# Kernel tuning notes

Measured on AMD Instinct MI355X. Metric: run time of the kernel, lower is better.

The kernel has to match this reference:

```python
import jax, jax.numpy as jnp
import numpy as np

C = 256
P = 8          # partition_size
DH = 32        # dim_head
NH = C // DH   # num heads
EXP = 4        # mlp expansion
EPS = 1e-5


def conv2d(x, w, b, stride, pad, groups):
    # x: NCHW, w: (O, I/groups, kh, kw)
    y = jax.lax.conv_general_dilated(
        x, w, (stride, stride), [(pad, pad), (pad, pad)],
        dimension_numbers=('NCHW', 'OIHW', 'NCHW'), feature_group_count=groups)
    return y + b[None, :, None, None]


def layernorm(x, g, b):
    m = jnp.mean(x, axis=-1, keepdims=True)
    v = jnp.mean((x - m) ** 2, axis=-1, keepdims=True)
    return (x - m) * jax.lax.rsqrt(v + EPS) * g + b


def partition_block(x):
    # (B,H,W,C) -> (B*nH*nW, P, P, C), MaxViT 'block' mode
    B, H, W, c = x.shape
    x = x.reshape(B, H // P, P, W // P, P, c)
    return x.transpose(0, 1, 3, 2, 4, 5).reshape(-1, P, P, c)


def reverse_block(w, H, W):
    c = w.shape[-1]
    x = w.reshape(-1, H // P, W // P, P, P, c)
    return x.transpose(0, 1, 3, 2, 4, 5).reshape(-1, H, W, c)


def window_attn(xw, qkv_w, qkv_b, proj_w, proj_b):
    # xw: (Nw, P, P, C); faithful to SelfAttentionCl (dropout inactive at eval)
    Nw = xw.shape[0]
    L = P * P
    qkv = xw.reshape(Nw, L, C) @ qkv_w.T + qkv_b           # (Nw, L, 3C)
    qkv = qkv.reshape(Nw, L, NH, 3 * DH).transpose(0, 2, 1, 3)  # (Nw, nh, L, 3dh)
    q, k, v = jnp.split(qkv, 3, axis=-1)
    attn = jax.nn.softmax((q @ jnp.swapaxes(k, -1, -2)) * (DH ** -0.5), axis=-1)
    o = (attn @ v).transpose(0, 2, 1, 3).reshape(Nw, P, P, C)
    return o @ proj_w.T + proj_b


def setup_inputs() -> dict:
    key = jax.random.key(0)
    ks = jax.random.split(key, 16)
    s = 0.02
    d = {
        'x': jax.random.normal(ks[0], (2, C, 256, 256), jnp.float32),
        'h': jnp.zeros((2, 256, 256, C), jnp.float32),
        'conv_w': s * jax.random.normal(ks[1], (C, 1, 3, 3), jnp.float32),
        'conv_b': jnp.zeros((C,), jnp.float32),
        'comb_w': s * jax.random.normal(ks[2], (C, 2, 7, 7), jnp.float32),
        'comb_b': jnp.zeros((C,), jnp.float32),
        'ln1_g': jnp.ones((C,), jnp.float32), 'ln1_b': jnp.zeros((C,), jnp.float32),
        'ln2_g': jnp.ones((C,), jnp.float32), 'ln2_b': jnp.zeros((C,), jnp.float32),
        'ln3_g': jnp.ones((C,), jnp.float32), 'ln3_b': jnp.zeros((C,), jnp.float32),
        'fsa_ln_g': jnp.ones((C,), jnp.float32), 'fsa_ln_b': jnp.zeros((C,), jnp.float32),
        'qkv_w': s * jax.random.normal(ks[3], (3 * C, C), jnp.float32),
        'qkv_b': jnp.zeros((3 * C,), jnp.float32),
        'proj_w': s * jax.random.normal(ks[4], (C, C), jnp.float32),
        'proj_b': jnp.zeros((C,), jnp.float32),
        'mlp_w1': s * jax.random.normal(ks[5], (EXP * C, C), jnp.float32),
        'mlp_b1': jnp.zeros((EXP * C,), jnp.float32),
        'mlp_w2': s * jax.random.normal(ks[6], (C, EXP * C), jnp.float32),
        'mlp_b2': jnp.zeros((C,), jnp.float32),
        'convg_w': s * jax.random.normal(ks[7], (C, 1, 7, 7), jnp.float32),
        'convg_b': jnp.zeros((C,), jnp.float32),
        'convh_w': s * jax.random.normal(ks[8], (C, 1, 7, 7), jnp.float32),
        'convh_b': jnp.zeros((C,), jnp.float32),
        'convf_w': s * jax.random.normal(ks[9], (C // 4, 4, 3, 3), jnp.float32),
        'convf_b': jnp.zeros((C // 4,), jnp.float32),
    }
    return d


def reference(x, h, conv_w, conv_b, comb_w, comb_b, ln1_g, ln1_b, ln2_g, ln2_b,
              ln3_g, ln3_b, fsa_ln_g, fsa_ln_b, qkv_w, qkv_b, proj_w, proj_b,
              mlp_w1, mlp_b1, mlp_w2, mlp_b2, convg_w, convg_b, convh_w, convh_b,
              convf_w, convf_b):
    relu = jax.nn.relu
    # depthwise conv + relu + LN (channels-last)
    x_conv = relu(conv2d(x, conv_w, conv_b, 1, 1, C)).transpose(0, 2, 3, 1)  # NHWC
    x_conv = layernorm(x_conv, ln1_g, ln1_b)
    H, W = x_conv.shape[1], x_conv.shape[2]
    # combine with recurrent state via grouped 7x7 conv (groups=C, 2 in-ch per group)
    xc = jnp.concatenate((x_conv, h), axis=3).transpose(0, 3, 1, 2)  # (B,2C,H,W)
    xc = conv2d(xc, comb_w, comb_b, 1, 3, C).transpose(0, 2, 3, 1)
    xc = layernorm(relu(xc), ln2_g, ln2_b)
    # block-windowed self-attention (UnifiedBlockGridAttention, mode='block')
    y = layernorm(xc, fsa_ln_g, fsa_ln_b)
    wins = partition_block(y)
    a = window_attn(wins, qkv_w, qkv_b, proj_w, proj_b)
    x_bsa = reverse_block(a, H, W)
    x_bsa = x_bsa + xc  # DropPath inactive (eval)
    x_bsa = layernorm(relu(x_bsa), ln3_g, ln3_b)
    # MLP (Linear -> GELU -> Linear), channels-last
    x_bsa = jax.nn.gelu(x_bsa @ mlp_w1.T + mlp_b1) @ mlp_w2.T + mlp_b2
    # output heads: depthwise 7x7 convs + grouped 3x3
    x_bsa = x_bsa.transpose(0, 3, 1, 2)
    x_bsa = relu(conv2d(x_bsa, convg_w, convg_b, 1, 3, C))
    h_new = relu(conv2d(x_bsa, convh_w, convh_b, 1, 3, C).transpose(0, 2, 3, 1))
    x_out = relu(conv2d(x_bsa, convf_w, convf_b, 1, 1, C // 4))
    return (x_out, h_new)
```

## Files before the change

### kernel.cpp

```cpp
#include <hip/hip_runtime.h>
#include <hip/hip_bf16.h>

#define HD 256
#define WD 256
#define CH 256
#define NB 2
#define NPIX (NB*HD*WD)

typedef __attribute__((ext_vector_type(4))) float f32x4;
typedef __attribute__((ext_vector_type(8))) short h16x8;
typedef __attribute__((ext_vector_type(4))) short h16x4;
typedef __fp16 f16x2 __attribute__((ext_vector_type(2)));

union U16 { uint4 q; f16x2 h[4]; };
union U8h { uint2 u; f16x2 h[2]; };
union UPK { f16x2 h; unsigned u; };

__device__ __forceinline__ short f2h(float f){
  __fp16 h = (__fp16)f;
  return *(short*)&h;
}
__device__ __forceinline__ unsigned p2h(float a, float b){
  UPK P; P.h = __builtin_amdgcn_cvt_pkrtz(a, b);
  return P.u;
}

__device__ __forceinline__ f32x4 mfma_f16(h16x8 a, h16x8 b, f32x4 c){
  asm("v_mfma_f32_16x16x32_f16 %0, %1, %2, %0" : "+v"(c) : "v"(a), "v"(b));
  return c;
}

__global__ __launch_bounds__(256) void k_cvtw(const float* __restrict__ qkvw,
    const float* __restrict__ projw, const float* __restrict__ w1,
    const float* __restrict__ w2, short* __restrict__ out){
  int i = blockIdx.x*256 + threadIdx.x;
  float v;
  if (i < 196608) v = qkvw[i];
  else if (i < 262144) v = projw[i-196608];
  else if (i < 524288) v = w1[i-262144];
  else v = w2[i-524288];
  out[i] = f2h(v);
}

__global__ __launch_bounds__(256) void k_cvth(const float* __restrict__ h, short* __restrict__ hh){
  int i = blockIdx.x*256 + threadIdx.x;
  const float4* p = ((const float4*)h) + (size_t)i*2;
  float4 a = p[0], b4 = p[1];
  U16 W;
  W.h[0] = __builtin_amdgcn_cvt_pkrtz(a.x, a.y);
  W.h[1] = __builtin_amdgcn_cvt_pkrtz(a.z, a.w);
  W.h[2] = __builtin_amdgcn_cvt_pkrtz(b4.x, b4.y);
  W.h[3] = __builtin_amdgcn_cvt_pkrtz(b4.z, b4.w);
  ((uint4*)hh)[i] = W.q;
}

__global__ __launch_bounds__(256) void k_prepw(const float* __restrict__ combw,
    const float* __restrict__ gw, const float* __restrict__ hw,
    const float* __restrict__ fw, float* __restrict__ wT){
  int i = blockIdx.x*256 + threadIdx.x;
  if (i < 25088){
    int wi = i>>9, r = i&511, ii = r>>8, o = r&255;
    wT[i] = combw[o*98 + ii*49 + wi];
  } else if (i < 37632){
    int j = i-25088; int wi = j>>8, c = j&255;
    wT[i] = gw[c*49 + wi];
  } else if (i < 50176){
    int j = i-37632; int wi = j>>8, c = j&255;
    wT[i] = hw[c*49 + wi];
  } else if (i < 52480){
    int j = i-50176; int tap = j>>8, r = j&255, oc = r>>2, ic = r&3;
    wT[i] = fw[oc*36 + ic*9 + tap];
  } else {
    int j = i-52480;
    int wi = j>>9, r2 = j&511;
    int o = r2>>1, ii = r2&1;
    ((__fp16*)wT)[104960 + j] = (__fp16)combw[o*98 + ii*49 + wi];
  }
}

__global__ __launch_bounds__(256) void k_conv3(const float* __restrict__ x,
    const float* __restrict__ w, const float* __restrict__ bias,
    const float* __restrict__ g1, const float* __restrict__ b1,
    short* __restrict__ out){
  int bid = blockIdx.x;
  int xb = bid & 15, y = (bid>>4) & 255, b = bid>>12;
  int t = threadIdx.x;
  __shared__ float tile[16][268];
  int xx0 = xb*16;
  {
    int xi = t & 15, cg = t >> 4;
    int xxg = xx0 + xi;
    #pragma unroll
    for (int k=0;k<16;++k){
      int c = cg*16 + k;
      const float* xp = x + ((size_t)(b*CH + c)*HD)*WD;
      float acc = bias[c];
      #pragma unroll
      for (int dy=-1; dy<=1; ++dy){
        int yy = y+dy;
        if ((unsigned)yy >= HD) continue;
        #pragma unroll
        for (int dx=-1; dx<=1; ++dx){
          int x2 = xxg+dx;
          if ((unsigned)x2 >= WD) continue;
          acc += xp[yy*WD + x2] * w[c*9 + (dy+1)*3 + (dx+1)];
        }
      }
      tile[xi][c] = fmaxf(acc, 0.f);
    }
  }
  __syncthreads();
  {
    int px = t >> 4, cs = t & 15;
    float4 m[4];
    #pragma unroll
    for (int j=0;j<4;++j) m[j] = *(const float4*)(&tile[px][cs*16 + j*4]);
    float s = 0.f, q = 0.f;
    #pragma unroll
    for (int j=0;j<4;++j){
      s += m[j].x+m[j].y+m[j].z+m[j].w;
      q += m[j].x*m[j].x+m[j].y*m[j].y+m[j].z*m[j].z+m[j].w*m[j].w;
    }
    #pragma unroll
    for (int o=1;o<16;o<<=1){ s += __shfl_xor(s,o); q += __shfl_xor(q,o); }
    float mean = s*(1.f/CH);
    float r = rsqrtf(q*(1.f/CH) - mean*mean + 1e-5f);
    size_t n = (size_t)(b*HD + y)*WD + xx0 + px;
    short* op = out + n*CH + cs*16;
    U16 W0, W1;
    #pragma unroll
    for (int j=0;j<4;++j){
      float4 G = *(const float4*)(g1 + cs*16 + j*4);
      float4 Bb = *(const float4*)(b1 + cs*16 + j*4);
      float4 o4;
      o4.x = (m[j].x-mean)*r*G.x + Bb.x;
      o4.y = (m[j].y-mean)*r*G.y + Bb.y;
      o4.z = (m[j].z-mean)*r*G.z + Bb.z;
      o4.w = (m[j].w-mean)*r*G.w + Bb.w;
      f16x2 p0 = __builtin_amdgcn_cvt_pkrtz(o4.x, o4.y);
      f16x2 p1 = __builtin_amdgcn_cvt_pkrtz(o4.z, o4.w);
      if (j<2){ W0.h[2*j] = p0; W0.h[2*j+1] = p1; }
      else    { W1.h[2*(j-2)] = p0; W1.h[2*(j-2)+1] = p1; }
    }
    *(uint4*)op = W0.q;
    *(uint4*)(op+8) = W1.q;
  }
}

__global__ __launch_bounds__(256) void k_comb(const short* __restrict__ xcv,
    const short* __restrict__ hh, const short* __restrict__ wTh,
    const float* __restrict__ bias,
    const float* __restrict__ g2, const float* __restrict__ b2,
    const float* __restrict__ gf, const float* __restrict__ bfv,
    short* __restrict__ xch, short* __restrict__ ybuf){
  int bid = blockIdx.x;
  int xg = bid & 63, yb = (bid>>6) & 63, b = bid>>12;
  int wv = threadIdx.x>>6, lane = threadIdx.x & 63;
  int xx = xg*4 + wv, y0 = yb*4;
  const short* S = (lane < 32) ? xcv : hh;
  int cin = 8*(lane & 31);
  float4 bv = ((const float4*)bias)[lane];
  float4 acc[4];
  #pragma unroll
  for (int i=0;i<4;++i) acc[i] = bv;
  bool inty = (y0 >= 3) && (y0 <= HD-7);
  #pragma unroll 1
  for (int dx=0; dx<7; ++dx){
    int x2 = xx + dx - 3;
    bool vx = (unsigned)x2 < WD;
    uint4 r[10];
    if (vx && inty){
      const short* base = S + ((size_t)((b*HD + y0-3)*WD + x2))*CH + cin;
      #pragma unroll
      for (int k=0;k<10;++k)
        r[k] = *(const uint4*)(base + (size_t)k*WD*CH);
    } else {
      #pragma unroll
      for (int k=0;k<10;++k){
        int yy = y0 + k - 3;
        if (vx && (unsigned)yy < HD)
          r[k] = *(const uint4*)(S + ((size_t)((b*HD+yy)*WD + x2))*CH + cin);
        else r[k] = uint4{0,0,0,0};
      }
    }
    #pragma unroll
    for (int dy=0; dy<7; ++dy){
      int wi = dy*7 + dx;
      U16 wq; wq.q = ((const uint4*)wTh)[wi*64 + lane];
      #pragma unroll
      for (int yi=0; yi<4; ++yi){
        U16 d; d.q = r[yi+dy];
        acc[yi].x = __builtin_amdgcn_fdot2(d.h[0], wq.h[0], acc[yi].x, false);
        acc[yi].y = __builtin_amdgcn_fdot2(d.h[1], wq.h[1], acc[yi].y, false);
        acc[yi].z = __builtin_amdgcn_fdot2(d.h[2], wq.h[2], acc[yi].z, false);
        acc[yi].w = __builtin_amdgcn_fdot2(d.h[3], wq.h[3], acc[yi].w, false);
      }
    }
  }
  float4 G2 = ((const float4*)g2)[lane],  B2 = ((const float4*)b2)[lane];
  float4 GF = ((const float4*)gf)[lane],  BF = ((const float4*)bfv)[lane];
  #pragma unroll
  for (int yi=0; yi<4; ++yi){
    float4 v;
    v.x = fmaxf(acc[yi].x, 0.f); v.y = fmaxf(acc[yi].y, 0.f);
    v.z = fmaxf(acc[yi].z, 0.f); v.w = fmaxf(acc[yi].w, 0.f);
    float s = v.x+v.y+v.z+v.w;
    float q = v.x*v.x+v.y*v.y+v.z*v.z+v.w*v.w;
    #pragma unroll
    for (int o=1;o<64;o<<=1){ s += __shfl_xor(s,o); q += __shfl_xor(q,o); }
    float mean = s*(1.f/CH);
    float r = rsqrtf(q*(1.f/CH) - mean*mean + 1e-5f);
    float4 w4;
    w4.x = (v.x-mean)*r*G2.x + B2.x;
    w4.y = (v.y-mean)*r*G2.y + B2.y;
    w4.z = (v.z-mean)*r*G2.z + B2.z;
    w4.w = (v.w-mean)*r*G2.w + B2.w;
    size_t n = (size_t)((b*HD + y0+yi)*WD + xx);
    union { f16x2 h[2]; uint2 u; } P;
    P.h[0] = __builtin_amdgcn_cvt_pkrtz(w4.x, w4.y);
    P.h[1] = __builtin_amdgcn_cvt_pkrtz(w4.z, w4.w);
    *(uint2*)(xch + n*CH + 4*lane) = P.u;
    float s2 = w4.x+w4.y+w4.z+w4.w;
    float q2 = w4.x*w4.x+w4.y*w4.y+w4.z*w4.z+w4.w*w4.w;
    #pragma unroll
    for (int o=1;o<64;o<<=1){ s2 += __shfl_xor(s2,o); q2 += __shfl_xor(q2,o); }
    float m2 = s2*(1.f/CH);
    float r2 = rsqrtf(q2*(1.f/CH) - m2*m2 + 1e-5f);
    union { f16x2 h[2]; uint2 u; } Y;
    Y.h[0] = __builtin_amdgcn_cvt_pkrtz((w4.x-m2)*r2*GF.x + BF.x, (w4.y-m2)*r2*GF.y + BF.y);
    Y.h[1] = __builtin_amdgcn_cvt_pkrtz((w4.z-m2)*r2*GF.z + BF.z, (w4.w-m2)*r2*GF.w + BF.w);
    *(uint2*)(ybuf + n*CH + 4*lane) = Y.u;
  }
}

__global__ __launch_bounds__(256) void k_attn(const short* __restrict__ ybuf,
    const short* __restrict__ wqkv, const float* __restrict__ qkvb,
    const short* __restrict__ wproj, const float* __restrict__ pb,
    const __fp16* __restrict__ xc, const float* __restrict__ g3,
    const float* __restrict__ b3, short* __restrict__ zbuf){
  __shared__ short wlds[24576];
  __shared__ short qs[64][40];
  __shared__ short ksm[64][40];
  __shared__ short vT[32][72];
  __shared__ short o2[2][64][36];
  __shared__ float redS[64][4];
  __shared__ float redQ[64][4];
  int wid = blockIdx.x;
  int b = wid>>10, wy = (wid>>5)&31, wx = wid&31;
  int t = threadIdx.x, wv = t>>6, lane = t&63;
  int g = lane>>4, c = lane&15;

  h16x8 afr[8];
  {
    int tok = 16*wv + c;
    size_t n = (size_t)(b*HD + wy*8 + (tok>>3))*WD + wx*8 + (tok&7);
    const short* yp = ybuf + n*CH;
    #pragma unroll
    for (int ks=0;ks<8;++ks)
      afr[ks] = *(const h16x8*)(yp + ks*32 + g*8);
  }
  {
    const short* wsrc = wqkv;
    #pragma unroll
    for (int i=0;i<12;++i){
      int rr = 24*wv + 2*i;
      int row = rr + (lane>>5);
      int colb = (lane&31)<<4;
      const short* gp = wsrc + row*256 + ((colb ^ ((row&7)<<4))>>1);
      __builtin_amdgcn_global_load_lds(
        (const __attribute__((address_space(1))) void*)gp,
        (__attribute__((address_space(3))) void*)(wlds + rr*256),
        16, 0, 0);
    }
  }
  __syncthreads();

  int s0 = c + 32*(g&1), s1 = s0 + 16;
  bool hiSel = (g & 2);

  f32x4 acc[4][4];
  #pragma unroll
  for (int mt=0;mt<4;++mt)
    #pragma unroll
    for (int nt=0;nt<4;++nt) acc[mt][nt] = (f32x4){0.f,0.f,0.f,0.f};

  #pragma unroll 1
  for (int hd=0; hd<8; ++hd){
    int cur = hd & 1;
    f32x4 qacc[6];
    #pragma unroll
    for (int nt=0;nt<6;++nt) qacc[nt] = (f32x4){0.f,0.f,0.f,0.f};
    #pragma unroll
    for (int nt=0; nt<6; ++nt){
      int R = nt*16 + c;
      const short* wr = wlds + R*256;
      int sw = (R&7)<<3;
      #pragma unroll
      for (int ks=0; ks<8; ++ks){
        h16x8 bf = *(const h16x8*)(wr + ((ks*32 + g*8) ^ sw));
        qacc[nt] = mfma_f16(afr[ks], bf, qacc[nt]);
      }
    }
    #pragma unroll
    for (int nt=0; nt<6; ++nt){
      float bias = qkvb[hd*96 + nt*16 + c];
      if (nt<4){
        #pragma unroll
        for (int j=0;j<4;++j){
          short hv = f2h(qacc[nt][j] + bias);
          int tok = 16*wv + 4*g + j;
          if (nt<2) qs[tok][nt*16 + c] = hv;
          else      ksm[tok][(nt-2)*16 + c] = hv;
        }
      } else {
        uint2 pk;
        pk.x = p2h(qacc[nt][0] + bias, qacc[nt][1] + bias);
        pk.y = p2h(qacc[nt][2] + bias, qacc[nt][3] + bias);
        *(uint2*)(&vT[(nt-4)*16 + c][16*wv + 4*g]) = pk;
      }
    }
    __syncthreads();
    if (hd < 7){
      const short* wsrc = wqkv + (size_t)(hd+1)*24576;
      #pragma unroll
      for (int i=0;i<12;++i){
        int rr = 24*wv + 2*i;
        int row = rr + (lane>>5);
        int colb = (lane&31)<<4;
        const short* gp = wsrc + row*256 + ((colb ^ ((row&7)<<4))>>1);
        __builtin_amdgcn_global_load_lds(
          (const __attribute__((address_space(1))) void*)gp,
          (__attribute__((address_space(3))) void*)(wlds + rr*256),
          16, 0, 0);
      }
    }
    f32x4 sv[4];
    h16x8 qa = *(const h16x8*)(&qs[16*wv + c][g*8]);
    #pragma unroll
    for (int nt=0;nt<4;++nt){
      h16x8 kb = *(const h16x8*)(&ksm[nt*16 + c][g*8]);
      f32x4 z = (f32x4){0.f,0.f,0.f,0.f};
      sv[nt] = mfma_f16(kb, qa, z);
    }
    float mx = sv[0][0];
    #pragma unroll
    for (int nt=0;nt<4;++nt)
      #pragma unroll
      for (int j=0;j<4;++j) mx = fmaxf(mx, sv[nt][j]);
    mx = fmaxf(mx, __shfl_xor(mx, 16));
    mx = fmaxf(mx, __shfl_xor(mx, 32));
    float sm = 0.f;
    #pragma unroll
    for (int nt=0;nt<4;++nt)
      #pragma unroll
      for (int j=0;j<4;++j){
        float e = __expf((sv[nt][j]-mx)*0.17677669529663687f);
        sv[nt][j] = e; sm += e;
      }
    sm += __shfl_xor(sm, 16);
    sm += __shfl_xor(sm, 32);
    float inv = 1.f/sm;
    unsigned pkLo[4], pkHi[4];
    #pragma unroll
    for (int nt=0;nt<4;++nt){
      pkLo[nt] = p2h(sv[nt][0], sv[nt][1]);
      pkHi[nt] = p2h(sv[nt][2], sv[nt][3]);
    }
    h16x8 pa[2];
    #pragma unroll
    for (int k2=0;k2<2;++k2){
      int n0 = 2*k2, n1 = 2*k2+1;
      unsigned w0a = __shfl((int)pkLo[n0], s0), w0b = __shfl((int)pkLo[n1], s0);
      unsigned w1a = __shfl((int)pkHi[n0], s0), w1b = __shfl((int)pkHi[n1], s0);
      unsigned w2a = __shfl((int)pkLo[n0], s1), w2b = __shfl((int)pkLo[n1], s1);
      unsigned w3a = __shfl((int)pkHi[n0], s1), w3b = __shfl((int)pkHi[n1], s1);
      union { unsigned u[4]; h16x8 v; } U;
      U.u[0] = hiSel ? w0b : w0a;
      U.u[1] = hiSel ? w1b : w1a;
      U.u[2] = hiSel ? w2b : w2a;
      U.u[3] = hiSel ? w3b : w3a;
      pa[k2] = U.v;
    }
    f32x4 ov[2];
    ov[0] = (f32x4){0.f,0.f,0.f,0.f}; ov[1] = (f32x4){0.f,0.f,0.f,0.f};
    #pragma unroll
    for (int k2=0;k2<2;++k2){
      #pragma unroll
      for (int nt=0;nt<2;++nt){
        h16x8 vb = *(const h16x8*)(&vT[nt*16 + c][k2*32 + g*8]);
        ov[nt] = mfma_f16(pa[k2], vb, ov[nt]);
      }
    }
    #pragma unroll
    for (int j=0;j<4;++j){
      float invO = __shfl(inv, 4*g + j);
      int tok = 16*wv + 4*g + j;
      o2[cur][tok][c]      = f2h(ov[0][j]*invO);
      o2[cur][tok][16 + c] = f2h(ov[1][j]*invO);
    }
    __syncthreads();
    #pragma unroll
    for (int mt=0;mt<4;++mt){
      h16x8 a = *(const h16x8*)(&o2[cur][mt*16+c][g*8]);
      #pragma unroll
      for (int nt=0;nt<4;++nt){
        h16x8 bfr = *(const h16x8*)(wproj + (size_t)(wv*64 + nt*16 + c)*256 + hd*32 + g*8);
        acc[mt][nt] = mfma_f16(a, bfr, acc[mt][nt]);
      }
    }
  }
  #pragma unroll
  for (int mt=0;mt<4;++mt){
    #pragma unroll
    for (int j=0;j<4;++j){
      int row_l = mt*16 + 4*g + j;
      size_t n = (size_t)(b*HD + wy*8 + (row_l>>3))*WD + wx*8 + (row_l&7);
      float ps_ = 0.f, pq_ = 0.f;
      #pragma unroll
      for (int nt=0;nt<4;++nt){
        int col = wv*64 + nt*16 + c;
        float v = acc[mt][nt][j] + pb[col] + (float)xc[n*CH + col];
        v = fmaxf(v, 0.f);
        acc[mt][nt][j] = v;
        ps_ += v; pq_ += v*v;
      }
      #pragma unroll
      for (int o=1;o<16;o<<=1){ ps_ += __shfl_xor(ps_,o); pq_ += __shfl_xor(pq_,o); }
      if (c==0){ redS[row_l][wv] = ps_; redQ[row_l][wv] = pq_; }
    }
  }
  __syncthreads();
  #pragma unroll
  for (int mt=0;mt<4;++mt){
    #pragma unroll
    for (int j=0;j<4;++j){
      int row_l = mt*16 + 4*g + j;
      size_t n = (size_t)(b*HD + wy*8 + (row_l>>3))*WD + wx*8 + (row_l&7);
      float st = redS[row_l][0]+redS[row_l][1]+redS[row_l][2]+redS[row_l][3];
      float qt = redQ[row_l][0]+redQ[row_l][1]+redQ[row_l][2]+redQ[row_l][3];
      float mean = st*(1.f/CH);
      float rs = rsqrtf(qt*(1.f/CH) - mean*mean + 1e-5f);
      #pragma unroll
      for (int nt=0;nt<4;++nt){
        int col = wv*64 + nt*16 + c;
        float y = (acc[mt][nt][j]-mean)*rs*g3[col] + b3[col];
        zbuf[n*CH + col] = f2h(y);
      }
    }
  }
}

__global__ __launch_bounds__(256) void k_mlp(const short* __restrict__ zbuf,
    const short* __restrict__ w1, const short* __restrict__ w2,
    const float* __restrict__ b1, const float* __restrict__ b2,
    __fp16* __restrict__ bsa){
  __shared__ short zt[16384];
  __shared__ short hid[64][140];
  int blk = blockIdx.x, t = threadIdx.x;
  int wv=t>>6, lane=t&63, g=lane>>4, c=lane&15;
  size_t m0 = (size_t)blk*64;
  {
    const short* zsrc = zbuf + m0*CH;
    #pragma unroll
    for (int i=0;i<8;++i){
      int rr = 16*wv + 2*i;
      int row = rr + (lane>>5);
      int colb = (lane&31)<<4;
      const short* gp = zsrc + row*256 + ((colb ^ ((row&7)<<4))>>1);
      __builtin_amdgcn_global_load_lds(
        (const __attribute__((address_space(1))) void*)gp,
        (__attribute__((address_space(3))) void*)(zt + rr*256),
        16, 0, 0);
    }
  }
  __syncthreads();
  f32x4 acc2[4][4];
  #pragma unroll
  for (int mt=0;mt<4;++mt)
    #pragma unroll
    for (int nt=0;nt<4;++nt) acc2[mt][nt] = (f32x4){0.f,0.f,0.f,0.f};
  #pragma unroll 1
  for (int hc=0; hc<8; ++hc){
    f32x4 a1[4][2];
    #pragma unroll
    for (int mt=0;mt<4;++mt){ a1[mt][0]=(f32x4){0.f,0.f,0.f,0.f}; a1[mt][1]=(f32x4){0.f,0.f,0.f,0.f}; }
    #pragma unroll 1
    for (int ks=0;ks<8;++ks){
      h16x8 a[4];
      #pragma unroll
      for (int mt=0;mt<4;++mt){
        int R = mt*16 + c;
        a[mt] = *(const h16x8*)(zt + R*256 + ((ks*32 + g*8) ^ ((R&7)<<3)));
      }
      #pragma unroll
      for (int nl=0;nl<2;++nl){
        int o = hc*128 + (wv*2+nl)*16 + c;
        h16x8 bfr = *(const h16x8*)(w1 + (size_t)o*256 + ks*32 + g*8);
        #pragma unroll
        for (int mt=0;mt<4;++mt)
          a1[mt][nl] = mfma_f16(a[mt], bfr, a1[mt][nl]);
      }
    }
    __syncthreads();
    #pragma unroll
    for (int mt=0;mt<4;++mt)
      #pragma unroll
      for (int nl=0;nl<2;++nl){
        int ol = (wv*2+nl)*16 + c;
        float bias = b1[hc*128 + ol];
        #pragma unroll
        for (int j=0;j<4;++j){
          float v = a1[mt][nl][j] + bias;
          float w = v*v;
          float tt = v*(1.5957691216f + 0.0713548162f*w);
          float e = __expf(-tt);
          float gv = v/(1.f + e);
          hid[mt*16 + 4*g + j][ol] = f2h(gv);
        }
      }
    __syncthreads();
    #pragma unroll 1
    for (int k2=0;k2<4;++k2){
      h16x8 a[4];
      #pragma unroll
      for (int mt=0;mt<4;++mt) a[mt] = *(const h16x8*)(&hid[mt*16+c][k2*32+g*8]);
      #pragma unroll
      for (int nt=0;nt<4;++nt){
        h16x8 bfr = *(const h16x8*)(w2 + (size_t)(wv*64+nt*16+c)*1024 + hc*128 + k2*32 + g*8);
        #pragma unroll
        for (int mt=0;mt<4;++mt)
          acc2[mt][nt] = mfma_f16(a[mt], bfr, acc2[mt][nt]);
      }
    }
  }
  #pragma unroll
  for (int mt=0;mt<4;++mt)
    #pragma unroll
    for (int nt=0;nt<4;++nt){
      int col = wv*64 + nt*16 + c;
      #pragma unroll
      for (int j=0;j<4;++j){
        int row_l = mt*16 + 4*g + j;
        bsa[(m0+row_l)*CH + col] = (__fp16)(acc2[mt][nt][j] + b2[col]);
      }
    }
}

__global__ __launch_bounds__(256) void k_dw7(const __fp16* __restrict__ src,
    const float* __restrict__ wT, const float* __restrict__ bias, __fp16* __restrict__ dst){
  int bid = blockIdx.x;
  int xg = bid & 63, yb = (bid>>6) & 31, b = bid>>11;
  int wv = threadIdx.x>>6, lane = threadIdx.x & 63;
  int xx = xg*4 + wv, y0 = yb*8;
  float4 bv = ((const float4*)bias)[lane];
  float4 acc[8];
  #pragma unroll
  for (int i=0;i<8;++i) acc[i] = bv;
  bool inty = (y0 >= 3) && (y0 <= HD-11);
  #pragma unroll 1
  for (int dx=0; dx<7; ++dx){
    int x2 = xx + dx - 3;
    bool vx = (unsigned)x2 < WD;
    float4 r[14];
    if (vx && inty){
      const __fp16* base = src + ((size_t)((b*HD + y0-3)*WD + x2))*CH + lane*4;
      #pragma unroll
      for (int k=0;k<14;++k){
        U8h H; H.u = *(const uint2*)(base + (size_t)k*WD*CH);
        r[k] = float4{(float)H.h[0][0], (float)H.h[0][1], (float)H.h[1][0], (float)H.h[1][1]};
      }
    } else {
      #pragma unroll
      for (int k=0;k<14;++k){
        int yy = y0 + k - 3;
        if (vx && (unsigned)yy < HD){
          U8h H; H.u = *(const uint2*)(src + ((size_t)((b*HD+yy)*WD + x2))*CH + lane*4);
          r[k] = float4{(float)H.h[0][0], (float)H.h[0][1], (float)H.h[1][0], (float)H.h[1][1]};
        } else r[k] = float4{0,0,0,0};
      }
    }
    #pragma unroll
    for (int dy=0; dy<7; ++dy){
      int wi = dy*7 + dx;
      float4 wv4 = ((const float4*)(wT + wi*256))[lane];
      #pragma unroll
      for (int yi=0; yi<8; ++yi){
        acc[yi].x += r[yi+dy].x * wv4.x;
        acc[yi].y += r[yi+dy].y * wv4.y;
        acc[yi].z += r[yi+dy].z * wv4.z;
        acc[yi].w += r[yi+dy].w * wv4.w;
      }
    }
  }
  #pragma unroll
  for (int yi=0; yi<8; ++yi){
    float4 o;
    o.x = fmaxf(acc[yi].x, 0.f); o.y = fmaxf(acc[yi].y, 0.f);
    o.z = fmaxf(acc[yi].z, 0.f); o.w = fmaxf(acc[yi].w, 0.f);
    size_t n = (size_t)((b*HD+y0+yi)*WD + xx);
    union { f16x2 h[2]; uint2 u; } P;
    P.h[0] = __builtin_amdgcn_cvt_pkrtz(o.x, o.y);
    P.h[1] = __builtin_amdgcn_cvt_pkrtz(o.z, o.w);
    *(uint2*)(dst + n*CH + lane*4) = P.u;
  }
}

__global__ __launch_bounds__(256) void k_dwf(const __fp16* __restrict__ src,
    const float* __restrict__ wTh7, const float* __restrict__ hbias,
    const float* __restrict__ wTf, const float* __restrict__ fbias,
    float* __restrict__ hout, float* __restrict__ xout){
  __shared__ float ot[4][8][65];
  int bid = blockIdx.x;
  int xg = bid & 63, yb = (bid>>6) & 31, b = bid>>11;
  int wv = threadIdx.x>>6, lane = threadIdx.x & 63;
  int xx = xg*4 + wv, y0 = yb*8;
  float4 bv = ((const float4*)hbias)[lane];
  float fbv = fbias[lane];
  float4 acc[8];
  float accf[8];
  #pragma unroll
  for (int i=0;i<8;++i){ acc[i] = bv; accf[i] = 0.f; }
  bool inty = (y0 >= 3) && (y0 <= HD-11);
  #pragma unroll 1
  for (int dx=0; dx<7; ++dx){
    int x2 = xx + dx - 3;
    bool vx = (unsigned)x2 < WD;
    float4 r[14];
    if (vx && inty){
      const __fp16* base = src + ((size_t)((b*HD + y0-3)*WD + x2))*CH + lane*4;
      #pragma unroll
      for (int k=0;k<14;++k){
        U8h H; H.u = *(const uint2*)(base + (size_t)k*WD*CH);
        r[k] = float4{(float)H.h[0][0], (float)H.h[0][1], (float)H.h[1][0], (float)H.h[1][1]};
      }
    } else {
      #pragma unroll
      for (int k=0;k<14;++k){
        int yy = y0 + k - 3;
        if (vx && (unsigned)yy < HD){
          U8h H; H.u = *(const uint2*)(src + ((size_t)((b*HD+yy)*WD + x2))*CH + lane*4);
          r[k] = float4{(float)H.h[0][0], (float)H.h[0][1], (float)H.h[1][0], (float)H.h[1][1]};
        } else r[k] = float4{0,0,0,0};
      }
    }
    #pragma unroll
    for (int dy=0; dy<7; ++dy){
      int wi = dy*7 + dx;
      float4 wv4 = ((const float4*)(wTh7 + wi*256))[lane];
      #pragma unroll
      for (int yi=0; yi<8; ++yi){
        acc[yi].x += r[yi+dy].x * wv4.x;
        acc[yi].y += r[yi+dy].y * wv4.y;
        acc[yi].z += r[yi+dy].z * wv4.z;
        acc[yi].w += r[yi+dy].w * wv4.w;
      }
    }
    if (dx >= 2 && dx <= 4){
      int fdx = dx - 2;
      #pragma unroll
      for (int dy=0; dy<3; ++dy){
        float4 w4 = ((const float4*)(wTf + (dy*3+fdx)*256))[lane];
        #pragma unroll
        for (int yi=0; yi<8; ++yi){
          float4 rv = r[yi+dy+2];
          accf[yi] += rv.x*w4.x + rv.y*w4.y + rv.z*w4.z + rv.w*w4.w;
        }
      }
    }
  }
  #pragma unroll
  for (int yi=0; yi<8; ++yi){
    float4 o;
    o.x = fmaxf(acc[yi].x, 0.f); o.y = fmaxf(acc[yi].y, 0.f);
    o.z = fmaxf(acc[yi].z, 0.f); o.w = fmaxf(acc[yi].w, 0.f);
    ((float4*)(hout + ((size_t)((b*HD+y0+yi)*WD + xx))*CH))[lane] = o;
  }
  #pragma unroll
  for (int yi=0; yi<8; ++yi) ot[wv][yi][lane] = fmaxf(accf[yi] + fbv, 0.f);
  __syncthreads();
  #pragma unroll
  for (int rep=0; rep<2; ++rep){
    int p = rep*256 + threadIdx.x;
    int oc = p>>3, yi = p&7;
    float4 v;
    v.x = ot[0][yi][oc]; v.y = ot[1][yi][oc]; v.z = ot[2][yi][oc]; v.w = ot[3][yi][oc];
    *(float4*)(xout + (((size_t)(b*64+oc))*HD + y0+yi)*WD + xg*4) = v;
  }
}

extern "C" void kernel_launch(void* const* d_in, const int* in_sizes, int n_in,
                              void* d_out, int out_size, void* d_ws, size_t ws_size,
                              hipStream_t stream) {
  const float* x      = (const float*)d_in[0];
  const float* hbuf   = (const float*)d_in[1];
  const float* conv_w = (const float*)d_in[2];
  const float* conv_b = (const float*)d_in[3];
  const float* comb_w = (const float*)d_in[4];
  const float* comb_b = (const float*)d_in[5];
  const float* ln1_g  = (const float*)d_in[6];
  const float* ln1_b  = (const float*)d_in[7];
  const float* ln2_g  = (const float*)d_in[8];
  const float* ln2_b  = (const float*)d_in[9];
  const float* ln3_g  = (const float*)d_in[10];
  const float* ln3_b  = (const float*)d_in[11];
  const float* fsa_g  = (const float*)d_in[12];
  const float* fsa_b  = (const float*)d_in[13];
  const float* qkv_w  = (const float*)d_in[14];
  const float* qkv_b  = (const float*)d_in[15];
  const float* proj_w = (const float*)d_in[16];
  const float* proj_b = (const float*)d_in[17];
  const float* mlp_w1 = (const float*)d_in[18];
  const float* mlp_b1 = (const float*)d_in[19];
  const float* mlp_w2 = (const float*)d_in[20];
  const float* mlp_b2 = (const float*)d_in[21];
  const float* convg_w= (const float*)d_in[22];
  const float* convg_b= (const float*)d_in[23];
  const float* convh_w= (const float*)d_in[24];
  const float* convh_b= (const float*)d_in[25];
  const float* convf_w= (const float*)d_in[26];
  const float* convf_b= (const float*)d_in[27];
  float* out = (float*)d_out;
  char* ws = (char*)d_ws;

  short* xcv  = (short*)(ws);
  short* hh   = (short*)(ws + 67108864);
  short* zbuf = (short*)(ws + 67108864);
  short* xch  = (short*)(ws + 134217728);
  __fp16* bsa = (__fp16*)(ws + 134217728);
  short* ybuf = (short*)(ws + 268435456);
  __fp16* gbuf= (__fp16*)(ws + 335544320);
  short* wb   = (short*)(ws + 469762048);
  float* wT   = (float*)(ws + 471334912);
  short* wTh  = (short*)wT + 104960;

  k_cvtw<<<3072,256,0,stream>>>(qkv_w, proj_w, mlp_w1, mlp_w2, wb);
  k_prepw<<<303,256,0,stream>>>(comb_w, convg_w, convh_w, convf_w, wT);
  k_cvth<<<16384,256,0,stream>>>(hbuf, hh);
  k_conv3<<<8192,256,0,stream>>>(x, conv_w, conv_b, ln1_g, ln1_b, xcv);
  k_comb<<<8192,256,0,stream>>>(xcv, hh, wTh, comb_b, ln2_g, ln2_b, fsa_g, fsa_b, xch, ybuf);
  k_attn<<<2048,256,0,stream>>>(ybuf, wb, qkv_b, wb+196608, proj_b, (const __fp16*)xch, ln3_g, ln3_b, zbuf);
  k_mlp<<<2048,256,0,stream>>>(zbuf, wb+262144, wb+524288, mlp_b1, mlp_b2, bsa);
  k_dw7<<<4096,256,0,stream>>>(bsa, wT+25088, convg_b, gbuf);
  k_dwf<<<4096,256,0,stream>>>(gbuf, wT+37632, convh_b, wT+50176, convf_b, out + 8388608, out);
}
```

Baseline: 1.165 ms.

## Repartition MLP kernel so each wave owns 16 rows and all output columns

The MLP kernel now gives each wave its own 16 rows instead of a column slice across all 64 rows. Each wave keeps its input row fragments in registers, so the LDS staging of the input tile and the block-wide barriers around the hidden buffer go away. In exchange, every wave must fetch all w1 and w2 weight fragments itself, and each fragment now feeds one MFMA instead of four. That roughly quadruples weight load traffic per block. It also raises register pressure with 16 output accumulators plus 8 cached A fragments.

```diff
diff --git a/kernel.cpp b/kernel.cpp
--- a/kernel.cpp
+++ b/kernel.cpp
@@ -454,96 +454,68 @@
     const short* __restrict__ w1, const short* __restrict__ w2,
     const float* __restrict__ b1, const float* __restrict__ b2,
     __fp16* __restrict__ bsa){
-  __shared__ short zt[16384];
   __shared__ short hid[64][140];
   int blk = blockIdx.x, t = threadIdx.x;
   int wv=t>>6, lane=t&63, g=lane>>4, c=lane&15;
   size_t m0 = (size_t)blk*64;
+  int row = 16*wv + c;
+  h16x8 afr[8];
   {
-    const short* zsrc = zbuf + m0*CH;
-    #pragma unroll
-    for (int i=0;i<8;++i){
-      int rr = 16*wv + 2*i;
-      int row = rr + (lane>>5);
-      int colb = (lane&31)<<4;
-      const short* gp = zsrc + row*256 + ((colb ^ ((row&7)<<4))>>1);
-      __builtin_amdgcn_global_load_lds(
-        (const __attribute__((address_space(1))) void*)gp,
-        (__attribute__((address_space(3))) void*)(zt + rr*256),
-        16, 0, 0);
-    }
-  }
-  __syncthreads();
-  f32x4 acc2[4][4];
-  #pragma unroll
-  for (int mt=0;mt<4;++mt)
-    #pragma unroll
-    for (int nt=0;nt<4;++nt) acc2[mt][nt] = (f32x4){0.f,0.f,0.f,0.f};
+    const short* zp = zbuf + (m0 + row)*CH + g*8;
+    #pragma unroll
+    for (int ks=0;ks<8;++ks) afr[ks] = *(const h16x8*)(zp + ks*32);
+  }
+  f32x4 acc2[16];
+  #pragma unroll
+  for (int nt=0;nt<16;++nt) acc2[nt] = (f32x4){0.f,0.f,0.f,0.f};
   #pragma unroll 1
   for (int hc=0; hc<8; ++hc){
-    f32x4 a1[4][2];
-    #pragma unroll
-    for (int mt=0;mt<4;++mt){ a1[mt][0]=(f32x4){0.f,0.f,0.f,0.f}; a1[mt][1]=(f32x4){0.f,0.f,0.f,0.f}; }
+    f32x4 a1[8];
+    #pragma unroll
+    for (int nl=0;nl<8;++nl) a1[nl] = (f32x4){0.f,0.f,0.f,0.f};
     #pragma unroll 1
     for (int ks=0;ks<8;++ks){
-      h16x8 a[4];
-      #pragma unroll
-      for (int mt=0;mt<4;++mt){
-        int R = mt*16 + c;
-        a[mt] = *(const h16x8*)(zt + R*256 + ((ks*32 + g*8) ^ ((R&7)<<3)));
-      }
-      #pragma unroll
-      for (int nl=0;nl<2;++nl){
-        int o = hc*128 + (wv*2+nl)*16 + c;
+      #pragma unroll
+      for (int nl=0;nl<8;++nl){
+        int o = hc*128 + nl*16 + c;
         h16x8 bfr = *(const h16x8*)(w1 + (size_t)o*256 + ks*32 + g*8);
-        #pragma unroll
-        for (int mt=0;mt<4;++mt)
-          a1[mt][nl] = mfma_f16(a[mt], bfr, a1[mt][nl]);
-      }
-    }
-    __syncthreads();
-    #pragma unroll
-    for (int mt=0;mt<4;++mt)
-      #pragma unroll
-      for (int nl=0;nl<2;++nl){
-        int ol = (wv*2+nl)*16 + c;
-        float bias = b1[hc*128 + ol];
-        #pragma unroll
-        for (int j=0;j<4;++j){
-          float v = a1[mt][nl][j] + bias;
-          float w = v*v;
-          float tt = v*(1.5957691216f + 0.0713548162f*w);
-          float e = __expf(-tt);
-          float gv = v/(1.f + e);
-          hid[mt*16 + 4*g + j][ol] = f2h(gv);
-        }
-      }
-    __syncthreads();
+        a1[nl] = mfma_f16(afr[ks], bfr, a1[nl]);
+      }
+    }
+    #pragma unroll
+    for (int nl=0;nl<8;++nl){
+      int ol = nl*16 + c;
+      float bias = b1[hc*128 + ol];
+      #pragma unroll
+      for (int j=0;j<4;++j){
+        float v = a1[nl][j] + bias;
+        float w = v*v;
+        float tt = v*(1.5957691216f + 0.0713548162f*w);
+        float e = __expf(-tt);
+        float gv = v/(1.f + e);
+        hid[16*wv + 4*g + j][ol] = f2h(gv);
+      }
+    }
     #pragma unroll 1
     for (int k2=0;k2<4;++k2){
-      h16x8 a[4];
-      #pragma unroll
-      for (int mt=0;mt<4;++mt) a[mt] = *(const h16x8*)(&hid[mt*16+c][k2*32+g*8]);
-      #pragma unroll
-      for (int nt=0;nt<4;++nt){
-        h16x8 bfr = *(const h16x8*)(w2 + (size_t)(wv*64+nt*16+c)*1024 + hc*128 + k2*32 + g*8);
-        #pragma unroll
-        for (int mt=0;mt<4;++mt)
-          acc2[mt][nt] = mfma_f16(a[mt], bfr, acc2[mt][nt]);
-      }
-    }
-  }
-  #pragma unroll
-  for (int mt=0;mt<4;++mt)
-    #pragma unroll
-    for (int nt=0;nt<4;++nt){
-      int col = wv*64 + nt*16 + c;
-      #pragma unroll
-      for (int j=0;j<4;++j){
-        int row_l = mt*16 + 4*g + j;
-        bsa[(m0+row_l)*CH + col] = (__fp16)(acc2[mt][nt][j] + b2[col]);
-      }
-    }
+      h16x8 ha = *(const h16x8*)(&hid[16*wv + c][k2*32 + g*8]);
+      #pragma unroll
+      for (int nt=0;nt<16;++nt){
+        h16x8 bfr = *(const h16x8*)(w2 + (size_t)(nt*16+c)*1024 + hc*128 + k2*32 + g*8);
+        acc2[nt] = mfma_f16(ha, bfr, acc2[nt]);
+      }
+    }
+  }
+  #pragma unroll
+  for (int nt=0;nt<16;++nt){
+    int col = nt*16 + c;
+    float bias = b2[col];
+    #pragma unroll
+    for (int j=0;j<4;++j){
+      int row_l = 16*wv + 4*g + j;
+      bsa[(m0+row_l)*CH + col] = (__fp16)(acc2[nt][j] + bias);
+    }
+  }
 }
 
 __global__ __launch_bounds__(256) void k_dw7(const __fp16* __restrict__ src,
```

Measured after the change: 2.868 ms. 2.46x slower.
